# Optimization experiments

Measured on AMD Instinct MI355X. Metric: run time of the kernel, lower is better.

The kernel has to match this reference:

```python
import jax, jax.numpy as jnp
import numpy as np

CH_IN, CH_OUT, CH, NLAYERS = 40, 9, 64, 10
CH_CLOSE = 2 * CH
KSZ = 9  # stencil hard-coded to 9 in init_weights
H = 0.1


def conv1(X, Ker):
    # F.conv1d(X, Ker, padding=(k-1)//2); Ker: (Cout, Cin, k)
    pad = (Ker.shape[-1] - 1) // 2
    return jax.lax.conv_general_dilated(X, Ker, (1,), [(pad, pad)],
                                        dimension_numbers=('NCH', 'OIH', 'NCH'))


def conv1T(X, Ker):
    # F.conv_transpose1d(X, Ker, padding=(k-1)//2) with stride 1 ==
    # conv1d with swapped in/out channels and flipped taps, padding k-1-(k-1)//2
    k = Ker.shape[-1]
    pad = k - 1 - (k - 1) // 2
    Kt = jnp.flip(jnp.swapaxes(Ker, 0, 1), -1)
    return jax.lax.conv_general_dilated(X, Kt, (1,), [(pad, pad)],
                                        dimension_numbers=('NCH', 'OIH', 'NCH'))


def mean_masked(X, mask, axis, keepdims=False):
    return jnp.sum(X * mask, axis=axis, keepdims=keepdims) / jnp.sum(mask, axis=axis, keepdims=keepdims)


def tr2dist(Y):
    # pairwise distances of columns of Y (B,C,N) -> (B,N,N), per Pfold tr2DistSmall
    k = Y.shape[1]
    Z = Y - jnp.mean(Y, axis=2, keepdims=True)
    n2 = jnp.sum(Z * Z, axis=1)  # (B,N)
    D = n2[:, :, None] + n2[:, None, :] - 2.0 * jnp.einsum('bcn,bcm->bnm', Z, Z)
    D = 3.0 * D / k
    Dr = jnp.maximum(D, 0.0)
    safe = jnp.where(Dr > 0, Dr, 1.0)  # grad-safe sqrt
    return jnp.where(Dr > 0, jnp.sqrt(safe), 0.0)


def get_graph_lap(X, mask, sigma):
    # X: (B,C,N), mask: (B,1,N)
    mm = jnp.einsum('bci,bcj->bij', mask, mask)  # (B,N,N) pair mask
    msum = jnp.sum(mask, axis=2, keepdims=True)
    Xc = X - (jnp.sum(X * mask, axis=2, keepdims=True) / msum) * mask
    Xc = Xc / jnp.sqrt(jnp.sum(Xc * Xc, axis=2, keepdims=True) / msum + 1e-4)
    N = X.shape[2]
    pos = 0.5 * jnp.linspace(0.0, 1.0, N)[None, None, :] * mask  # (B,1,N)
    Xa = jnp.concatenate([Xc, pos], axis=1)
    W = tr2dist(Xa) * mm
    W = jnp.exp(-W / sigma * 10.0) * mm
    Wsum = jnp.sum(W, axis=1)  # (B,N)
    D = Wsum[:, :, None] * jnp.eye(N, dtype=W.dtype)  # diag(Wsum)
    L = D - W
    return 0.5 * (L + jnp.swapaxes(L, 1, 2)), W


def double_sym(Z, Wi, Bi, L, mask):
    A0 = conv1(Z + Bi[0], Wi[0]) * mask
    A0 = (A0 - mean_masked(A0, mask, 2, True)) * mask
    A0 = A0 / jnp.sqrt(jnp.sum(A0 * A0, axis=1, keepdims=True) + 1e-3)
    A1 = (conv1(Z + Bi[1], Wi[1]) @ L) * mask
    A1 = (A1 - mean_masked(A1, mask, 2, True)) * mask
    A1 = A1 / jnp.sqrt(jnp.sum(A1 * A1, axis=1, keepdims=True) + 1e-3)
    A0 = jax.nn.relu(A0)
    A1 = jax.nn.relu(A1)
    A0 = conv1T(A0, Wi[0]) * mask
    A1 = (conv1T(A1, Wi[1]) @ L) * mask
    return A0 + A1


def hypernet_forward(Z, mask, Kopen, Kclose, W, Bias):
    mask = mask[:, None, :]  # (B,1,N)
    Z = jnp.einsum('ci,bin->bcn', Kopen, Z) * mask
    L, _ = get_graph_lap(Z, mask, 10.0)
    for i in range(W.shape[0]):
        if i % 10 == 0:
            L, _ = get_graph_lap(Z, mask, 10.0)
        Z = Z - H * double_sym(Z, W[i], Bias[i], L, mask)
    Z = jnp.einsum('oc,bcn->bon', Kclose, Z) * mask
    dists = jnp.stack([tr2dist(Z[:, 3 * i:3 * i + 3, :]) for i in range(Z.shape[1] // 3)], axis=1)
    return dists, Z  # dists: (B, chan_out//3, N, N)


def setup_inputs() -> dict:
    key = jax.random.key(0)
    ks = jax.random.split(key, 5)
    B, N = 8, 1024
    Z = jax.random.normal(ks[0], (B, CH_IN, N), dtype=jnp.float32)
    mask = jnp.ones((B, N), dtype=jnp.float32)
    so = float(CH) / CH_IN
    Kopen = jax.random.uniform(ks[1], (CH, CH_IN), minval=-so, maxval=so, dtype=jnp.float32)
    sc = float(CH_OUT) / CH
    Kclose = jax.random.uniform(ks[2], (CH_OUT, CH), minval=-sc, maxval=sc, dtype=jnp.float32)
    W = jax.random.uniform(ks[3], (NLAYERS, 2, CH_CLOSE, CH, KSZ), minval=-0.1, maxval=0.1, dtype=jnp.float32)
    Bias = jax.random.uniform(ks[4], (NLAYERS, 2, CH, 1), dtype=jnp.float32) * 0.001
    return {"Z": Z, "mask": mask, "Kopen": Kopen, "Kclose": Kclose, "W": W, "Bias": Bias}


def reference(Z, mask, Kopen, Kclose, W, Bias):
    return hypernet_forward(Z, mask, Kopen, Kclose, W, Bias)
```

## Files before the change

### kernel.cpp

```cpp
#include <hip/hip_runtime.h>
#include <cstddef>

#define BB 8
#define NN 1024
#define CIN 40
#define CH 64
#define CC 128
#define COUT 9
#define KS 9
#define NL 10
#define HSTEP 0.1f
#define SKC 2
#define SKH 4

typedef __attribute__((ext_vector_type(8))) short bf16x8;
typedef __attribute__((ext_vector_type(4))) float f32x4;

__device__ __forceinline__ unsigned short f2bf(float f) {
    union { float f; unsigned u; } v;
    v.f = f;
    unsigned u = v.u;
    u += 0x7FFFu + ((u >> 16) & 1u);
    return (unsigned short)(u >> 16);
}
__device__ __forceinline__ float bf2f(unsigned short h) {
    union { unsigned u; float f; } v;
    v.u = ((unsigned)h) << 16;
    return v.f;
}

__device__ __forceinline__ size_t pk_addr(int lb, int row, int col, int R, int KDv) {
    int chunk = ((lb * (R / 32) + (row >> 5)) * (KDv / 32) + (col >> 5)) * 2 + ((row >> 4) & 1);
    int lane = ((col >> 3) & 3) * 16 + (row & 15);
    return ((size_t)chunk * 64 + lane) * 8 + (col & 7);
}

__device__ __forceinline__ float blockSum(float v, float* red) {
    int tid = threadIdx.x;
    red[tid] = v;
    __syncthreads();
    for (int s = 128; s > 0; s >>= 1) {
        if (tid < s) red[tid] += red[tid + s];
        __syncthreads();
    }
    float r = red[0];
    __syncthreads();
    return r;
}

__global__ __launch_bounds__(256) void k_prep_wbf(const float* __restrict__ Win,
                                                  unsigned short* __restrict__ PKc_h,
                                                  unsigned short* __restrict__ PKc_l,
                                                  unsigned short* __restrict__ PKt_h,
                                                  unsigned short* __restrict__ PKt_l) {
    int idx = blockIdx.x * 256 + threadIdx.x;
    const int total = NL * 2 * CC * CH * KS;
    if (idx >= total) return;
    int k = idx % KS;
    int t = idx / KS;
    int i = t % CH;  t /= CH;
    int o = t % CC;  t /= CC;
    int lb = t;
    float v = Win[idx];
    unsigned short h = f2bf(v);
    unsigned short l = f2bf(v - bf2f(h));
    size_t ac = pk_addr(lb, o, k * 64 + i, CC, 576);
    size_t at = pk_addr(lb, i, (8 - k) * 128 + o, CH, 1152);
    PKc_h[ac] = h;
    PKc_l[ac] = l;
    PKt_h[at] = h;
    PKt_l[at] = l;
}

__global__ __launch_bounds__(256) void k_wpack2(const float* __restrict__ Wg,
                                                unsigned short* __restrict__ dst) {
    int idx = blockIdx.x * 256 + threadIdx.x;
    int lane = idx & 63;
    int t = idx >> 6;
    int fn = t & 1; t >>= 1;
    int ms = t & 31; t >>= 5;
    int nt = t & 31;
    int b = t >> 5;
    int r = lane & 15, g = lane >> 4;
    const float* sp = &Wg[((size_t)b * NN + nt * 32 + fn * 16 + r) * NN + ms * 32 + g * 8];
    float v[8];
    *reinterpret_cast<float4*>(&v[0]) = *reinterpret_cast<const float4*>(sp);
    *reinterpret_cast<float4*>(&v[4]) = *reinterpret_cast<const float4*>(sp + 4);
    unsigned short* dp = dst + (size_t)idx * 8;
#pragma unroll
    for (int j = 0; j < 8; ++j) dp[j] = f2bf(v[j]);
}

__global__ __launch_bounds__(256) void k_prep_bks(const float* __restrict__ Win,
                                                  const float* __restrict__ Bias,
                                                  float* __restrict__ bks) {
    int idx = blockIdx.x * 256 + threadIdx.x;
    const int total = NL * 2 * CC * KS;
    if (idx >= total) return;
    int k = idx % KS;
    int t = idx / KS;
    int o = t % CC;
    int lb = t / CC;
    float s = 0.f;
    for (int i = 0; i < CH; ++i)
        s += Win[(((size_t)lb * CC + o) * CH + i) * KS + k] * Bias[lb * CH + i];
    bks[idx] = s;
}

__global__ __launch_bounds__(256) void k_open(const float* __restrict__ Zin,
                                              const float* __restrict__ mask,
                                              const float* __restrict__ Kop,
                                              float* __restrict__ Zcur) {
    int n = blockIdx.x * 256 + threadIdx.x;
    int c = blockIdx.y, b = blockIdx.z;
    float acc = 0.f;
    for (int i = 0; i < CIN; ++i)
        acc += Kop[c * CIN + i] * Zin[((size_t)b * CIN + i) * NN + n];
    Zcur[((size_t)b * CH + c) * NN + n] = acc * mask[b * NN + n];
}

__global__ __launch_bounds__(256) void k_za(const float* __restrict__ Zcur,
                                            const float* __restrict__ mask,
                                            float* __restrict__ Za) {
    __shared__ float red[256];
    int c = blockIdx.x;
    int b = blockIdx.y;
    int tid = threadIdx.x;
    const float* m = mask + b * NN;
    float x[4], mv[4];
    if (c < CH) {
        const float* src = Zcur + ((size_t)b * CH + c) * NN;
#pragma unroll
        for (int j = 0; j < 4; ++j) { int n = tid * 4 + j; x[j] = src[n]; mv[j] = m[n]; }
    } else {
#pragma unroll
        for (int j = 0; j < 4; ++j) { int n = tid * 4 + j; mv[j] = m[n]; x[j] = 0.5f * ((float)n / 1023.f) * mv[j]; }
    }
    float sm = 0.f, sxm = 0.f;
#pragma unroll
    for (int j = 0; j < 4; ++j) { sm += mv[j]; sxm += x[j] * mv[j]; }
    float msum = blockSum(sm, red);
    float xm = blockSum(sxm, red);
    if (c < CH) {
        float mean = xm / msum;
        float ss = 0.f;
#pragma unroll
        for (int j = 0; j < 4; ++j) { x[j] -= mean * mv[j]; ss += x[j] * x[j]; }
        ss = blockSum(ss, red);
        float sc = rsqrtf(ss / msum + 1e-4f);
#pragma unroll
        for (int j = 0; j < 4; ++j) x[j] *= sc;
    }
    float ps = 0.f;
#pragma unroll
    for (int j = 0; j < 4; ++j) ps += x[j];
    float pm = blockSum(ps, red) / (float)NN;
    float* dst = Za + ((size_t)b * 65 + c) * NN;
#pragma unroll
    for (int j = 0; j < 4; ++j) dst[tid * 4 + j] = x[j] - pm;
}

__global__ __launch_bounds__(256) void k_n2g(const float* __restrict__ Za, float* __restrict__ n2g) {
    int n = blockIdx.x * 256 + threadIdx.x;
    int b = blockIdx.y;
    float s = 0.f;
    for (int c = 0; c < 65; ++c) { float v = Za[((size_t)b * 65 + c) * NN + n]; s += v * v; }
    n2g[b * NN + n] = s;
}

__global__ __launch_bounds__(256) void k_gramW(const float* __restrict__ Za,
                                               const float* __restrict__ n2g,
                                               const float* __restrict__ mask,
                                               float* __restrict__ Wg) {
    __shared__ float As[65][64];
    __shared__ float Bs2[65][64];
    int i0 = blockIdx.x * 64, j0 = blockIdx.y * 64, b = blockIdx.z;
    int tid = threadIdx.x;
    for (int e = tid; e < 65 * 64; e += 256) {
        int c = e >> 6, t = e & 63;
        const float* src = Za + ((size_t)b * 65 + c) * NN;
        As[c][t] = src[i0 + t];
        Bs2[c][t] = src[j0 + t];
    }
    __syncthreads();
    int tx = tid & 15, ty = tid >> 4;
    float acc[4][4] = {};
    for (int c = 0; c < 65; ++c) {
        float a[4];
#pragma unroll
        for (int q = 0; q < 4; ++q) a[q] = As[c][ty * 4 + q];
        float bv[4];
        *reinterpret_cast<float4*>(bv) = *reinterpret_cast<const float4*>(&Bs2[c][tx * 4]);
#pragma unroll
        for (int q = 0; q < 4; ++q)
#pragma unroll
            for (int r = 0; r < 4; ++r) acc[q][r] += a[q] * bv[r];
    }
    const float* m = mask + b * NN;
    for (int q = 0; q < 4; ++q) {
        int i = i0 + ty * 4 + q;
        float n2i = n2g[b * NN + i], mi = m[i];
        float res[4];
#pragma unroll
        for (int r = 0; r < 4; ++r) {
            int j = j0 + tx * 4 + r;
            float D = n2i + n2g[b * NN + j] - 2.f * acc[q][r];
            D *= (3.f / 65.f);
            D = fmaxf(D, 0.f);
            float dist = (D > 0.f) ? sqrtf(D) : 0.f;
            float mmv = mi * m[j];
            res[r] = expf(-dist * mmv) * mmv;
        }
        *reinterpret_cast<float4*>(&Wg[((size_t)b * NN + i) * NN + j0 + tx * 4]) =
            *reinterpret_cast<float4*>(res);
    }
}

__global__ __launch_bounds__(256) void k_wsum_part(const float* __restrict__ Wg,
                                                   float* __restrict__ Wsp) {
    int j = blockIdx.x * 256 + threadIdx.x;
    int ch = blockIdx.y;
    int b = blockIdx.z;
    float s = 0.f;
    int i0 = ch * 64;
#pragma unroll 8
    for (int i = 0; i < 64; ++i) s += Wg[((size_t)b * NN + i0 + i) * NN + j];
    Wsp[((size_t)b * 16 + ch) * NN + j] = s;
}
__global__ __launch_bounds__(256) void k_wsum_fin(const float* __restrict__ Wsp,
                                                  float* __restrict__ Wsum) {
    int j = blockIdx.x * 256 + threadIdx.x;
    int b = blockIdx.y;
    float s = 0.f;
#pragma unroll
    for (int ch = 0; ch < 16; ++ch) s += Wsp[((size_t)b * 16 + ch) * NN + j];
    Wsum[b * NN + j] = s;
}

__global__ __launch_bounds__(256) void k_conv1_mfma(const float* __restrict__ Zcur,
                                                    const unsigned short* __restrict__ Wh,
                                                    const unsigned short* __restrict__ Wl,
                                                    const float* __restrict__ bksl,
                                                    const float* __restrict__ mask,
                                                    float* __restrict__ C0,
                                                    float* __restrict__ C1) {
    __shared__ __align__(16) unsigned short xh[80][64];
    __shared__ __align__(16) unsigned short xl[80][64];
    int n0 = blockIdx.x * 64;
    int y = blockIdx.y;
    int b = blockIdx.z;
    int br = y >> 1, half = y & 1;
    int tid = threadIdx.x;
    const float* Xb = Zcur + (size_t)b * CH * NN;

    for (int e = tid; e < 64 * 20; e += 256) {
        int i = e / 20, t = e - i * 20;
        int gn = n0 + t * 4 - 4;
        float4 v = make_float4(0.f, 0.f, 0.f, 0.f);
        if (gn >= 0 && gn + 3 < NN) v = *reinterpret_cast<const float4*>(&Xb[(size_t)i * NN + gn]);
        float vv[4] = {v.x, v.y, v.z, v.w};
#pragma unroll
        for (int j = 0; j < 4; ++j) {
            int row = t * 4 + j;
            int col = i ^ ((row & 7) << 3);
            unsigned short h = f2bf(vv[j]);
            xh[row][col] = h;
            xl[row][col] = f2bf(vv[j] - bf2f(h));
        }
    }
    __syncthreads();

    int wid = tid >> 6, lane = tid & 63;
    int wo = (wid >> 1) * 32, wn = (wid & 1) * 32;
    int r = lane & 15, g = lane >> 4;
    int r32 = half * 2 + (wid >> 1);
    size_t brOff = (size_t)br * (CC / 32) * (576 / 32) * 1024;

    f32x4 acc[2][2] = {};
#pragma unroll 3
    for (int q = 0; q < 18; ++q) {
        int k = q >> 1, s = q & 1;
        size_t widx = brOff + ((size_t)(r32 * 18 + q)) * 1024 + lane * 8;
        bf16x8 ah[2], al[2];
        ah[0] = *reinterpret_cast<const bf16x8*>(&Wh[widx]);
        ah[1] = *reinterpret_cast<const bf16x8*>(&Wh[widx + 512]);
        al[0] = *reinterpret_cast<const bf16x8*>(&Wl[widx]);
        al[1] = *reinterpret_cast<const bf16x8*>(&Wl[widx + 512]);
        bf16x8 bh[2], bl[2];
#pragma unroll
        for (int fn = 0; fn < 2; ++fn) {
            int row = wn + fn * 16 + r + k;
            int chs = (s * 32 + g * 8) ^ ((row & 7) << 3);
            bh[fn] = *reinterpret_cast<const bf16x8*>(&xh[row][chs]);
            bl[fn] = *reinterpret_cast<const bf16x8*>(&xl[row][chs]);
        }
#pragma unroll
        for (int fc = 0; fc < 2; ++fc)
#pragma unroll
            for (int fn = 0; fn < 2; ++fn) {
                acc[fc][fn] = __builtin_amdgcn_mfma_f32_16x16x32_bf16(ah[fc], bh[fn], acc[fc][fn], 0, 0, 0);
                acc[fc][fn] = __builtin_amdgcn_mfma_f32_16x16x32_bf16(al[fc], bh[fn], acc[fc][fn], 0, 0, 0);
                acc[fc][fn] = __builtin_amdgcn_mfma_f32_16x16x32_bf16(ah[fc], bl[fn], acc[fc][fn], 0, 0, 0);
            }
    }

    const float* mkB = mask + b * NN;
    float* Outp = (br ? C1 : C0) + ((size_t)b * CC + half * 64) * NN;
    const float* bo_base = bksl + (br * CC + half * 64) * KS;
#pragma unroll
    for (int fc = 0; fc < 2; ++fc) {
#pragma unroll
        for (int fn = 0; fn < 2; ++fn) {
            int n = n0 + wn + fn * 16 + r;
#pragma unroll
            for (int rr = 0; rr < 4; ++rr) {
                int oo = wo + fc * 16 + 4 * g + rr;
                float v = acc[fc][fn][rr];
                const float* bo = bo_base + oo * KS;
                float bias = 0.f;
#pragma unroll
                for (int k = 0; k < KS; ++k) {
                    int nn2 = n + k - 4;
                    if (nn2 >= 0 && nn2 < NN) bias += bo[k];
                }
                v += bias;
                if (br == 0) v *= mkB[n];
                Outp[(size_t)oo * NN + n] = v;
            }
        }
    }
}

__global__ __launch_bounds__(256) void k_convT_mfma(const float* __restrict__ C0,
                                                    const float* __restrict__ A1,
                                                    const unsigned short* __restrict__ Wh,
                                                    const unsigned short* __restrict__ Wl,
                                                    const float* __restrict__ mask,
                                                    const float* __restrict__ meanA,
                                                    const float* __restrict__ invA,
                                                    float* __restrict__ T0,
                                                    float* __restrict__ T1p) {
    __shared__ __align__(16) unsigned short xh[48][128];
    __shared__ __align__(16) unsigned short xl[48][128];
    __shared__ float red2[2][32][33];
    int n0 = blockIdx.x * 32;
    int br = blockIdx.y;
    int b = blockIdx.z;
    int tid = threadIdx.x;
    const float* Xb = (br ? A1 : C0) + (size_t)b * CC * NN;
    const float* meB = meanA + ((size_t)br * BB + b) * CC;
    const float* ivB = invA + ((size_t)br * BB + b) * NN;
    const float* mkB = mask + b * NN;

    for (int e = tid; e < 128 * 12; e += 256) {
        int i = e / 12, t = e - i * 12;
        int gn = n0 + t * 4 - 4;
        float4 v = make_float4(0.f, 0.f, 0.f, 0.f);
        if (gn >= 0 && gn + 3 < NN) {
            v = *reinterpret_cast<const float4*>(&Xb[(size_t)i * NN + gn]);
            float me = meB[i];
            float4 iv = *reinterpret_cast<const float4*>(&ivB[gn]);
            float4 mk = *reinterpret_cast<const float4*>(&mkB[gn]);
            v.x = fmaxf((v.x - me) * mk.x * iv.x, 0.f);
            v.y = fmaxf((v.y - me) * mk.y * iv.y, 0.f);
            v.z = fmaxf((v.z - me) * mk.z * iv.z, 0.f);
            v.w = fmaxf((v.w - me) * mk.w * iv.w, 0.f);
        }
        float vv[4] = {v.x, v.y, v.z, v.w};
#pragma unroll
        for (int j = 0; j < 4; ++j) {
            int row = t * 4 + j;
            int col = i ^ ((row & 7) << 3);
            unsigned short h = f2bf(vv[j]);
            xh[row][col] = h;
            xl[row][col] = f2bf(vv[j] - bf2f(h));
        }
    }
    __syncthreads();

    int wid = tid >> 6, lane = tid & 63;
    int i32 = wid & 1, kh = wid >> 1;
    int r = lane & 15, g = lane >> 4;
    size_t brW = (size_t)br * (CH / 32) * (1152 / 32) * 1024;

    f32x4 acc[2][2] = {};
#pragma unroll 3
    for (int t = 0; t < 18; ++t) {
        int k = t >> 1, s = kh * 2 + (t & 1);
        int q32 = k * 4 + s;
        size_t widx = brW + ((size_t)(i32 * 36 + q32)) * 1024 + lane * 8;
        bf16x8 ah[2], al[2];
        ah[0] = *reinterpret_cast<const bf16x8*>(&Wh[widx]);
        ah[1] = *reinterpret_cast<const bf16x8*>(&Wh[widx + 512]);
        al[0] = *reinterpret_cast<const bf16x8*>(&Wl[widx]);
        al[1] = *reinterpret_cast<const bf16x8*>(&Wl[widx + 512]);
        bf16x8 bh[2], bl[2];
#pragma unroll
        for (int fn = 0; fn < 2; ++fn) {
            int row = fn * 16 + r + k;
            int chs = (s * 32 + g * 8) ^ ((row & 7) << 3);
            bh[fn] = *reinterpret_cast<const bf16x8*>(&xh[row][chs]);
            bl[fn] = *reinterpret_cast<const bf16x8*>(&xl[row][chs]);
        }
#pragma unroll
        for (int fc = 0; fc < 2; ++fc)
#pragma unroll
            for (int fn = 0; fn < 2; ++fn) {
                acc[fc][fn] = __builtin_amdgcn_mfma_f32_16x16x32_bf16(ah[fc], bh[fn], acc[fc][fn], 0, 0, 0);
                acc[fc][fn] = __builtin_amdgcn_mfma_f32_16x16x32_bf16(al[fc], bh[fn], acc[fc][fn], 0, 0, 0);
                acc[fc][fn] = __builtin_amdgcn_mfma_f32_16x16x32_bf16(ah[fc], bl[fn], acc[fc][fn], 0, 0, 0);
            }
    }

    if (kh == 1) {
#pragma unroll
        for (int fc = 0; fc < 2; ++fc)
#pragma unroll
            for (int fn = 0; fn < 2; ++fn)
#pragma unroll
                for (int rr = 0; rr < 4; ++rr)
                    red2[i32][fc * 16 + 4 * g + rr][fn * 16 + r] = acc[fc][fn][rr];
    }
    __syncthreads();
    if (kh == 0) {
        float* Outp = (br ? T1p : T0) + (size_t)b * CH * NN;
#pragma unroll
        for (int fc = 0; fc < 2; ++fc)
#pragma unroll
            for (int fn = 0; fn < 2; ++fn) {
                int n = n0 + fn * 16 + r;
#pragma unroll
                for (int rr = 0; rr < 4; ++rr) {
                    int irow = fc * 16 + 4 * g + rr;
                    float v = acc[fc][fn][rr] + red2[i32][irow][fn * 16 + r];
                    Outp[(size_t)(i32 * 32 + irow) * NN + n] = v;
                }
            }
    }
}

template <int SKN>
__global__ __launch_bounds__(256) void k_matL_mfma(const float* __restrict__ X,
                                                   const unsigned short* __restrict__ Wpk,
                                                   float* __restrict__ Part, int rows) {
    __shared__ __align__(16) unsigned short Xs[64][36];
    int cb = rows >> 6;
    int n0 = blockIdx.x * 64;
    int sk = blockIdx.y;
    int b = blockIdx.z / cb;
    int c0 = (blockIdx.z % cb) * 64;
    int tid = threadIdx.x;
    int wid = tid >> 6, lane = tid & 63;
    int wc = (wid >> 1) * 32;
    int r = lane & 15, g = lane >> 4;
    const float* Xb = X + (size_t)b * rows * NN;
    int nt32 = blockIdx.x * 2 + (wid & 1);
    const unsigned short* Wb = Wpk + ((size_t)b * 32 + nt32) * 32 * 1024;

    int srow = tid >> 2, scol = (tid & 3) * 8;
    f32x4 acc[2][2] = {};
    int m_beg = sk * (NN / SKN);
    for (int m0 = m_beg; m0 < m_beg + NN / SKN; m0 += 32) {
        {
            const float* sp = &Xb[(size_t)(c0 + srow) * NN + m0 + scol];
            float v[8];
            *reinterpret_cast<float4*>(&v[0]) = *reinterpret_cast<const float4*>(sp);
            *reinterpret_cast<float4*>(&v[4]) = *reinterpret_cast<const float4*>(sp + 4);
            unsigned short h[8];
#pragma unroll
            for (int j = 0; j < 8; ++j) h[j] = f2bf(v[j]);
            *reinterpret_cast<ushort4*>(&Xs[srow][scol]) = *reinterpret_cast<ushort4*>(&h[0]);
            *reinterpret_cast<ushort4*>(&Xs[srow][scol + 4]) = *reinterpret_cast<ushort4*>(&h[4]);
        }
        __syncthreads();
        bf16x8 afr[2];
#pragma unroll
        for (int fc = 0; fc < 2; ++fc) {
            const uint2* p = reinterpret_cast<const uint2*>(&Xs[wc + fc * 16 + r][8 * g]);
            uint2 q0 = p[0], q1 = p[1];
            union { unsigned int u[4]; bf16x8 v; } ua;
            ua.u[0] = q0.x; ua.u[1] = q0.y; ua.u[2] = q1.x; ua.u[3] = q1.y;
            afr[fc] = ua.v;
        }
        size_t wb = (size_t)(m0 >> 5) * 1024 + lane * 8;
        bf16x8 bfr[2];
        bfr[0] = *reinterpret_cast<const bf16x8*>(&Wb[wb]);
        bfr[1] = *reinterpret_cast<const bf16x8*>(&Wb[wb + 512]);
#pragma unroll
        for (int fc = 0; fc < 2; ++fc)
#pragma unroll
            for (int fn = 0; fn < 2; ++fn)
                acc[fc][fn] = __builtin_amdgcn_mfma_f32_16x16x32_bf16(afr[fc], bfr[fn], acc[fc][fn], 0, 0, 0);
        __syncthreads();
    }
    int wn = (wid & 1) * 32;
#pragma unroll
    for (int fc = 0; fc < 2; ++fc)
#pragma unroll
        for (int fn = 0; fn < 2; ++fn) {
            int ncol = n0 + wn + fn * 16 + r;
#pragma unroll
            for (int rr = 0; rr < 4; ++rr) {
                int crow = c0 + wc + fc * 16 + 4 * g + rr;
                Part[(((size_t)b * SKN + sk) * rows + crow) * NN + ncol] = acc[fc][fn][rr];
            }
        }
}

template <int SKN, int MODE>
__global__ __launch_bounds__(256) void k_matL_fin(const float* __restrict__ X,
                                                  const float* __restrict__ Part,
                                                  const float* __restrict__ Wsum,
                                                  const float* __restrict__ mask,
                                                  const float* __restrict__ T0,
                                                  float* __restrict__ Out,
                                                  float* __restrict__ meanA, int rows) {
    __shared__ float red[256];
    int c = blockIdx.x, b = blockIdx.y;
    int n = threadIdx.x * 4;
    float4 s = make_float4(0.f, 0.f, 0.f, 0.f);
#pragma unroll
    for (int sk = 0; sk < SKN; ++sk) {
        float4 p = *reinterpret_cast<const float4*>(
            &Part[(((size_t)b * SKN + sk) * rows + c) * NN + n]);
        s.x += p.x; s.y += p.y; s.z += p.z; s.w += p.w;
    }
    float4 xv = *reinterpret_cast<const float4*>(&X[((size_t)b * rows + c) * NN + n]);
    float4 wv = *reinterpret_cast<const float4*>(&Wsum[b * NN + n]);
    float4 mv = *reinterpret_cast<const float4*>(&mask[b * NN + n]);
    float y0 = xv.x * wv.x - s.x, y1 = xv.y * wv.y - s.y;
    float y2 = xv.z * wv.z - s.z, y3 = xv.w * wv.w - s.w;
    if (MODE == 0) {
        float4 res = make_float4(y0 * mv.x, y1 * mv.y, y2 * mv.z, y3 * mv.w);
        *reinterpret_cast<float4*>(&Out[((size_t)b * rows + c) * NN + n]) = res;
        float rs = res.x * mv.x + res.y * mv.y + res.z * mv.z + res.w * mv.w;
        float ms = mv.x + mv.y + mv.z + mv.w;
        rs = blockSum(rs, red);
        ms = blockSum(ms, red);
        if (threadIdx.x == 0) meanA[((size_t)BB + b) * CC + c] = rs / ms;
    } else {
        float4 t0 = *reinterpret_cast<const float4*>(&T0[((size_t)b * rows + c) * NN + n]);
        float4 o = *reinterpret_cast<const float4*>(&Out[((size_t)b * rows + c) * NN + n]);
        float4 res = make_float4(o.x - HSTEP * mv.x * (t0.x + y0),
                                 o.y - HSTEP * mv.y * (t0.y + y1),
                                 o.z - HSTEP * mv.z * (t0.z + y2),
                                 o.w - HSTEP * mv.w * (t0.w + y3));
        *reinterpret_cast<float4*>(&Out[((size_t)b * rows + c) * NN + n]) = res;
    }
}

__global__ __launch_bounds__(256) void k_rowmean(const float* __restrict__ X0,
                                                 const float* __restrict__ mask,
                                                 float* __restrict__ meanA) {
    __shared__ float red[256];
    int c = blockIdx.x, b = blockIdx.y, tid = threadIdx.x;
    const float* src = X0 + ((size_t)b * CC + c) * NN;
    const float* m = mask + b * NN;
    float s = 0.f, sm = 0.f;
    for (int n = tid; n < NN; n += 256) { float mv = m[n]; s += src[n] * mv; sm += mv; }
    float ts = blockSum(s, red);
    float tm = blockSum(sm, red);
    if (tid == 0) meanA[(size_t)b * CC + c] = ts / tm;
}

__global__ __launch_bounds__(256) void k_colnorm_inv(const float* __restrict__ X0,
                                                     const float* __restrict__ X1,
                                                     const float* __restrict__ mask,
                                                     const float* __restrict__ meanA,
                                                     float* __restrict__ invA) {
    __shared__ float red[8][32];
    int tid = threadIdx.x;
    int nl = tid & 31, cg = tid >> 5;
    int n = blockIdx.x * 32 + nl;
    int b = blockIdx.y, z = blockIdx.z;
    const float* X = (z ? X1 : X0) + (size_t)b * CC * NN;
    const float* me = meanA + ((size_t)z * BB + b) * CC;
    float mv = mask[b * NN + n];
    float ss = 0.f;
#pragma unroll
    for (int cc = 0; cc < 16; ++cc) {
        int c = cg * 16 + cc;
        float v = (X[(size_t)c * NN + n] - me[c]) * mv;
        ss += v * v;
    }
    red[cg][nl] = ss;
    __syncthreads();
    if (cg < 4) red[cg][nl] += red[cg + 4][nl];
    __syncthreads();
    if (cg < 2) red[cg][nl] += red[cg + 2][nl];
    __syncthreads();
    if (cg < 1) red[0][nl] += red[1][nl];
    __syncthreads();
    if (cg == 0) invA[((size_t)z * BB + b) * NN + n] = rsqrtf(red[0][nl] + 0.001f);
}

__global__ __launch_bounds__(256) void k_close(const float* __restrict__ Zcur,
                                               const float* __restrict__ Kcl,
                                               const float* __restrict__ mask,
                                               float* __restrict__ Zout) {
    __shared__ float red[4][64][COUT];
    int tid = threadIdx.x;
    int nl = tid & 63, cg = tid >> 6;
    int n = blockIdx.x * 64 + nl;
    int b = blockIdx.y;
    float acc[COUT] = {};
#pragma unroll
    for (int cc = 0; cc < 16; ++cc) {
        int c = cg * 16 + cc;
        float zv = Zcur[((size_t)b * CH + c) * NN + n];
#pragma unroll
        for (int o = 0; o < COUT; ++o) acc[o] += Kcl[o * CH + c] * zv;
    }
#pragma unroll
    for (int o = 0; o < COUT; ++o) red[cg][nl][o] = acc[o];
    __syncthreads();
    if (cg == 0) {
        float mv = mask[b * NN + n];
#pragma unroll
        for (int o = 0; o < COUT; ++o) {
            float s = red[0][nl][o] + red[1][nl][o] + red[2][nl][o] + red[3][nl][o];
            Zout[((size_t)b * COUT + o) * NN + n] = s * mv;
        }
    }
}

__global__ __launch_bounds__(256) void k_center3(const float* __restrict__ Zout, float* __restrict__ Zc3) {
    __shared__ float red[256];
    int c = blockIdx.x, b = blockIdx.y, tid = threadIdx.x;
    const float* src = Zout + ((size_t)b * COUT + c) * NN;
    float s = 0.f;
    for (int n = tid; n < NN; n += 256) s += src[n];
    float mean = blockSum(s, red) / (float)NN;
    float* dst = Zc3 + ((size_t)b * COUT + c) * NN;
    for (int n = tid; n < NN; n += 256) dst[n] = src[n] - mean;
}

__global__ __launch_bounds__(256) void k_n23(const float* __restrict__ Zc3, float* __restrict__ n23) {
    int n = blockIdx.x * 256 + threadIdx.x;
    int g = blockIdx.y, b = blockIdx.z;
    float s = 0.f;
#pragma unroll
    for (int c = 0; c < 3; ++c) { float v = Zc3[((size_t)b * COUT + g * 3 + c) * NN + n]; s += v * v; }
    n23[((size_t)b * 3 + g) * NN + n] = s;
}

__global__ __launch_bounds__(256) void k_dist(const float* __restrict__ Zc3,
                                              const float* __restrict__ n23,
                                              float* __restrict__ dout) {
    __shared__ float Ai[3][64], Aj[3][64], ni[64], nj[64];
    int bg = blockIdx.z;
    int b = bg / 3, g = bg - 3 * b;
    int i0 = blockIdx.x * 64, j0 = blockIdx.y * 64;
    int tid = threadIdx.x;
    if (tid < 64) ni[tid] = n23[((size_t)b * 3 + g) * NN + i0 + tid];
    else if (tid < 128) { int t = tid - 64; nj[t] = n23[((size_t)b * 3 + g) * NN + j0 + t]; }
    for (int e = tid; e < 192; e += 256) {
        int c = e / 64, t = e - c * 64;
        Ai[c][t] = Zc3[((size_t)b * COUT + g * 3 + c) * NN + i0 + t];
    }
    for (int e = tid; e < 192; e += 256) {
        int c = e / 64, t = e - c * 64;
        Aj[c][t] = Zc3[((size_t)b * COUT + g * 3 + c) * NN + j0 + t];
    }
    __syncthreads();
    int tx = tid & 15, ty = tid >> 4;
    for (int q = 0; q < 4; ++q) {
        int i = ty * 4 + q;
        float a0 = Ai[0][i], a1 = Ai[1][i], a2 = Ai[2][i], n2i = ni[i];
        float res[4];
#pragma unroll
        for (int r = 0; r < 4; ++r) {
            int j = tx * 4 + r;
            float D = n2i + nj[j] - 2.f * (a0 * Aj[0][j] + a1 * Aj[1][j] + a2 * Aj[2][j]);
            D = fmaxf(D, 0.f);
            res[r] = (D > 0.f) ? sqrtf(D) : 0.f;
        }
        *reinterpret_cast<float4*>(&dout[(((size_t)b * 3 + g) * NN + i0 + i) * NN + j0 + tx * 4]) =
            *reinterpret_cast<float4*>(res);
    }
}

extern "C" void kernel_launch(void* const* d_in, const int* in_sizes, int n_in,
                              void* d_out, int out_size, void* d_ws, size_t ws_size,
                              hipStream_t stream) {
    (void)in_sizes; (void)n_in; (void)out_size; (void)ws_size;
    const float* Zin  = (const float*)d_in[0];
    const float* mask = (const float*)d_in[1];
    const float* Kop  = (const float*)d_in[2];
    const float* Kcl  = (const float*)d_in[3];
    const float* Win  = (const float*)d_in[4];
    const float* Bias = (const float*)d_in[5];
    float* out = (float*)d_out;
    float* ws = (float*)d_ws;

    size_t off = 0;
    float* Zcur = ws + off;  off += (size_t)BB * CH * NN;
    float* C0   = ws + off;  off += (size_t)BB * CC * NN;
    float* C1   = ws + off;  off += (size_t)BB * CC * NN;
    float* A1   = ws + off;  off += (size_t)BB * CC * NN;
    float* T0   = ws + off;  off += (size_t)BB * CH * NN;
    float* T1p  = ws + off;  off += (size_t)BB * CH * NN;
    float* Za   = ws + off;  off += (size_t)BB * 65 * NN;
    float* n2g  = ws + off;  off += (size_t)BB * NN;
    float* Wg   = ws + off;  off += (size_t)BB * NN * NN;
    float* Wsum = ws + off;  off += (size_t)BB * NN;
    float* meanA= ws + off;  off += (size_t)2 * BB * CC;
    float* bks  = ws + off;  off += (size_t)NL * 2 * CC * KS;
    float* Zc3  = ws + off;  off += (size_t)BB * COUT * NN;
    float* n23  = ws + off;  off += (size_t)BB * 3 * NN;
    float* Wsp  = ws + off;  off += (size_t)BB * 16 * NN;
    float* invA = ws + off;  off += (size_t)2 * BB * NN;

    float* Part = out;
    unsigned short* Wpk2  = (unsigned short*)(out + (size_t)4194304);
    unsigned short* PKc_h = (unsigned short*)(out + (size_t)14680064);
    unsigned short* PKc_l = (unsigned short*)(out + (size_t)15417344);
    unsigned short* PKt_h = (unsigned short*)(out + (size_t)16154624);
    unsigned short* PKt_l = (unsigned short*)(out + (size_t)16891904);

    const int wtot = NL * 2 * CC * CH * KS;
    k_prep_wbf<<<dim3((wtot + 255) / 256), 256, 0, stream>>>(Win, PKc_h, PKc_l, PKt_h, PKt_l);
    k_prep_bks<<<dim3((NL * 2 * CC * KS + 255) / 256), 256, 0, stream>>>(Win, Bias, bks);
    k_open<<<dim3(NN / 256, CH, BB), 256, 0, stream>>>(Zin, mask, Kop, Zcur);
    k_za<<<dim3(65, BB), 256, 0, stream>>>(Zcur, mask, Za);
    k_n2g<<<dim3(NN / 256, BB), 256, 0, stream>>>(Za, n2g);
    k_gramW<<<dim3(16, 16, BB), 256, 0, stream>>>(Za, n2g, mask, Wg);
    k_wsum_part<<<dim3(NN / 256, 16, BB), 256, 0, stream>>>(Wg, Wsp);
    k_wsum_fin<<<dim3(NN / 256, BB), 256, 0, stream>>>(Wsp, Wsum);
    k_wpack2<<<dim3((int)((size_t)BB * NN * NN / 8 / 256)), 256, 0, stream>>>(Wg, Wpk2);

    for (int l = 0; l < NL; ++l) {
        const unsigned short* PKc_h_l = PKc_h + (size_t)l * 2 * CC * 576;
        const unsigned short* PKc_l_l = PKc_l + (size_t)l * 2 * CC * 576;
        const unsigned short* PKt_h_l = PKt_h + (size_t)l * 2 * CH * 1152;
        const unsigned short* PKt_l_l = PKt_l + (size_t)l * 2 * CH * 1152;
        const float* bksl = bks + (size_t)l * 2 * CC * KS;

        k_conv1_mfma<<<dim3(NN / 64, 4, BB), 256, 0, stream>>>(
            Zcur, PKc_h_l, PKc_l_l, bksl, mask, C0, C1);
        k_matL_mfma<SKC><<<dim3(NN / 64, SKC, BB * (CC / 64)), 256, 0, stream>>>(C1, Wpk2, Part, CC);
        k_matL_fin<SKC, 0><<<dim3(CC, BB), 256, 0, stream>>>(
            C1, Part, Wsum, mask, nullptr, A1, meanA, CC);
        k_rowmean<<<dim3(CC, BB), 256, 0, stream>>>(C0, mask, meanA);
        k_colnorm_inv<<<dim3(NN / 32, BB, 2), 256, 0, stream>>>(C0, A1, mask, meanA, invA);
        k_convT_mfma<<<dim3(NN / 32, 2, BB), 256, 0, stream>>>(
            C0, A1, PKt_h_l, PKt_l_l, mask, meanA, invA, T0, T1p);
        k_matL_mfma<SKH><<<dim3(NN / 64, SKH, BB * (CH / 64)), 256, 0, stream>>>(T1p, Wpk2, Part, CH);
        k_matL_fin<SKH, 1><<<dim3(CH, BB), 256, 0, stream>>>(
            T1p, Part, Wsum, mask, T0, Zcur, nullptr, CH);
    }

    float* Zout = out + (size_t)BB * 3 * NN * NN;
    k_close<<<dim3(NN / 64, BB), 256, 0, stream>>>(Zcur, Kcl, mask, Zout);
    k_center3<<<dim3(COUT, BB), 256, 0, stream>>>(Zout, Zc3);
    k_n23<<<dim3(NN / 256, 3, BB), 256, 0, stream>>>(Zc3, n23);
    k_dist<<<dim3(16, 16, 3 * BB), 256, 0, stream>>>(Zc3, n23, out);
}
```

Before: 952.2 us.

## Fuse graph weight packing and column sums into gram kernel; prepack matL operands

The gram kernel now writes the bf16 MFMA-packed W matrix and accumulates column sums with atomics, instead of storing a full fp32 W and running separate wsum and pack kernels. The conv1 and convT kernels also emit bf16 fragment-packed copies of C1 and T1p, so matL loads its A-operand directly from global memory without LDS staging or syncs. This removes a 32MB fp32 write and read plus several launches, and makes the inner matL loop pure loads and MFMAs. In exchange there are extra scattered 2-byte stores in the conv epilogues, and atomic adds make the column-sum order nondeterministic.

```diff
diff --git a/kernel.cpp b/kernel.cpp
--- a/kernel.cpp
+++ b/kernel.cpp
@@ -46,6 +46,11 @@
     float r = red[0];
     __syncthreads();
     return r;
+}
+
+__global__ __launch_bounds__(256) void k_zero(float* __restrict__ p, int n) {
+    int i = blockIdx.x * 256 + threadIdx.x;
+    if (i < n) p[i] = 0.f;
 }
 
 __global__ __launch_bounds__(256) void k_prep_wbf(const float* __restrict__ Win,
@@ -72,25 +77,6 @@
     PKt_l[at] = l;
 }
 
-__global__ __launch_bounds__(256) void k_wpack2(const float* __restrict__ Wg,
-                                                unsigned short* __restrict__ dst) {
-    int idx = blockIdx.x * 256 + threadIdx.x;
-    int lane = idx & 63;
-    int t = idx >> 6;
-    int fn = t & 1; t >>= 1;
-    int ms = t & 31; t >>= 5;
-    int nt = t & 31;
-    int b = t >> 5;
-    int r = lane & 15, g = lane >> 4;
-    const float* sp = &Wg[((size_t)b * NN + nt * 32 + fn * 16 + r) * NN + ms * 32 + g * 8];
-    float v[8];
-    *reinterpret_cast<float4*>(&v[0]) = *reinterpret_cast<const float4*>(sp);
-    *reinterpret_cast<float4*>(&v[4]) = *reinterpret_cast<const float4*>(sp + 4);
-    unsigned short* dp = dst + (size_t)idx * 8;
-#pragma unroll
-    for (int j = 0; j < 8; ++j) dp[j] = f2bf(v[j]);
-}
-
 __global__ __launch_bounds__(256) void k_prep_bks(const float* __restrict__ Win,
                                                   const float* __restrict__ Bias,
                                                   float* __restrict__ bks) {
@@ -171,9 +157,12 @@
 __global__ __launch_bounds__(256) void k_gramW(const float* __restrict__ Za,
                                                const float* __restrict__ n2g,
                                                const float* __restrict__ mask,
-                                               float* __restrict__ Wg) {
+                                               unsigned short* __restrict__ Wpk,
+                                               float* __restrict__ Wsum) {
     __shared__ float As[65][64];
     __shared__ float Bs2[65][64];
+    __shared__ unsigned short wt[64][72];
+    __shared__ float csred[16][64];
     int i0 = blockIdx.x * 64, j0 = blockIdx.y * 64, b = blockIdx.z;
     int tid = threadIdx.x;
     for (int e = tid; e < 65 * 64; e += 256) {
@@ -197,10 +186,10 @@
             for (int r = 0; r < 4; ++r) acc[q][r] += a[q] * bv[r];
     }
     const float* m = mask + b * NN;
+    float csacc[4] = {0.f, 0.f, 0.f, 0.f};
     for (int q = 0; q < 4; ++q) {
         int i = i0 + ty * 4 + q;
         float n2i = n2g[b * NN + i], mi = m[i];
-        float res[4];
 #pragma unroll
         for (int r = 0; r < 4; ++r) {
             int j = j0 + tx * 4 + r;
@@ -209,32 +198,35 @@
             D = fmaxf(D, 0.f);
             float dist = (D > 0.f) ? sqrtf(D) : 0.f;
             float mmv = mi * m[j];
-            res[r] = expf(-dist * mmv) * mmv;
-        }
-        *reinterpret_cast<float4*>(&Wg[((size_t)b * NN + i) * NN + j0 + tx * 4]) =
-            *reinterpret_cast<float4*>(res);
-    }
-}
-
-__global__ __launch_bounds__(256) void k_wsum_part(const float* __restrict__ Wg,
-                                                   float* __restrict__ Wsp) {
-    int j = blockIdx.x * 256 + threadIdx.x;
-    int ch = blockIdx.y;
-    int b = blockIdx.z;
-    float s = 0.f;
-    int i0 = ch * 64;
-#pragma unroll 8
-    for (int i = 0; i < 64; ++i) s += Wg[((size_t)b * NN + i0 + i) * NN + j];
-    Wsp[((size_t)b * 16 + ch) * NN + j] = s;
-}
-__global__ __launch_bounds__(256) void k_wsum_fin(const float* __restrict__ Wsp,
-                                                  float* __restrict__ Wsum) {
-    int j = blockIdx.x * 256 + threadIdx.x;
-    int b = blockIdx.y;
-    float s = 0.f;
-#pragma unroll
-    for (int ch = 0; ch < 16; ++ch) s += Wsp[((size_t)b * 16 + ch) * NN + j];
-    Wsum[b * NN + j] = s;
+            float res = expf(-dist * mmv) * mmv;
+            wt[ty * 4 + q][tx * 4 + r] = f2bf(res);
+            csacc[r] += res;
+        }
+    }
+#pragma unroll
+    for (int r = 0; r < 4; ++r) csred[ty][tx * 4 + r] = csacc[r];
+    __syncthreads();
+    for (int s = 8; s > 0; s >>= 1) {
+        if (ty < s) {
+#pragma unroll
+            for (int r = 0; r < 4; ++r) csred[ty][tx * 4 + r] += csred[ty + s][tx * 4 + r];
+        }
+        __syncthreads();
+    }
+    if (ty == 0) {
+#pragma unroll
+        for (int r = 0; r < 4; ++r)
+            atomicAdd(&Wsum[b * NN + j0 + tx * 4 + r], csred[0][tx * 4 + r]);
+    }
+    for (int e = tid; e < 512; e += 256) {
+        int li = e >> 3, ljb = (e & 7) * 8;
+        int row = i0 + li, col = j0 + ljb;
+        int chunk = ((b * 32 + (row >> 5)) * 32 + (col >> 5)) * 2 + ((row >> 4) & 1);
+        int lane2 = ((col >> 3) & 3) * 16 + (row & 15);
+        unsigned short* dp = Wpk + ((size_t)chunk * 64 + lane2) * 8;
+        *reinterpret_cast<ushort4*>(dp) = *reinterpret_cast<ushort4*>(&wt[li][ljb]);
+        *reinterpret_cast<ushort4*>(dp + 4) = *reinterpret_cast<ushort4*>(&wt[li][ljb + 4]);
+    }
 }
 
 __global__ __launch_bounds__(256) void k_conv1_mfma(const float* __restrict__ Zcur,
@@ -243,7 +235,8 @@
                                                     const float* __restrict__ bksl,
                                                     const float* __restrict__ mask,
                                                     float* __restrict__ C0,
-                                                    float* __restrict__ C1) {
+                                                    float* __restrict__ C1,
+                                                    unsigned short* __restrict__ C1pk) {
     __shared__ __align__(16) unsigned short xh[80][64];
     __shared__ __align__(16) unsigned short xl[80][64];
     int n0 = blockIdx.x * 64;
@@ -326,6 +319,12 @@
                 v += bias;
                 if (br == 0) v *= mkB[n];
                 Outp[(size_t)oo * NN + n] = v;
+                if (br == 1) {
+                    int cg = half * 64 + oo;
+                    int chunk = ((b * 4 + (cg >> 5)) * 32 + (n >> 5)) * 2 + ((cg >> 4) & 1);
+                    int lane2 = ((n >> 3) & 3) * 16 + (cg & 15);
+                    C1pk[((size_t)chunk * 64 + lane2) * 8 + (n & 7)] = f2bf(v);
+                }
             }
         }
     }
@@ -339,7 +338,8 @@
                                                     const float* __restrict__ meanA,
                                                     const float* __restrict__ invA,
                                                     float* __restrict__ T0,
-                                                    float* __restrict__ T1p) {
+                                                    float* __restrict__ T1p,
+                                                    unsigned short* __restrict__ T1pk) {
     __shared__ __align__(16) unsigned short xh[48][128];
     __shared__ __align__(16) unsigned short xl[48][128];
     __shared__ float red2[2][32][33];
@@ -434,18 +434,22 @@
                     int irow = fc * 16 + 4 * g + rr;
                     float v = acc[fc][fn][rr] + red2[i32][irow][fn * 16 + r];
                     Outp[(size_t)(i32 * 32 + irow) * NN + n] = v;
+                    if (br == 1) {
+                        int cg = i32 * 32 + irow;
+                        int chunk = ((b * 2 + (cg >> 5)) * 32 + (n >> 5)) * 2 + ((cg >> 4) & 1);
+                        int lane2 = ((n >> 3) & 3) * 16 + (cg & 15);
+                        T1pk[((size_t)chunk * 64 + lane2) * 8 + (n & 7)] = f2bf(v);
+                    }
                 }
             }
     }
 }
 
 template <int SKN>
-__global__ __launch_bounds__(256) void k_matL_mfma(const float* __restrict__ X,
+__global__ __launch_bounds__(256) void k_matL_mfma(const unsigned short* __restrict__ Xpk,
                                                    const unsigned short* __restrict__ Wpk,
                                                    float* __restrict__ Part, int rows) {
-    __shared__ __align__(16) unsigned short Xs[64][36];
     int cb = rows >> 6;
-    int n0 = blockIdx.x * 64;
     int sk = blockIdx.y;
     int b = blockIdx.z / cb;
     int c0 = (blockIdx.z % cb) * 64;
@@ -453,46 +457,26 @@
     int wid = tid >> 6, lane = tid & 63;
     int wc = (wid >> 1) * 32;
     int r = lane & 15, g = lane >> 4;
-    const float* Xb = X + (size_t)b * rows * NN;
+    int rowsT = rows >> 5;
+    int ct = (c0 >> 5) + (wid >> 1);
     int nt32 = blockIdx.x * 2 + (wid & 1);
-    const unsigned short* Wb = Wpk + ((size_t)b * 32 + nt32) * 32 * 1024;
-
-    int srow = tid >> 2, scol = (tid & 3) * 8;
+    const unsigned short* Xb = Xpk + ((size_t)(b * rowsT + ct)) * 32768 + (size_t)lane * 8;
+    const unsigned short* Wb = Wpk + ((size_t)(b * 32 + nt32)) * 32768 + (size_t)lane * 8;
+
     f32x4 acc[2][2] = {};
-    int m_beg = sk * (NN / SKN);
-    for (int m0 = m_beg; m0 < m_beg + NN / SKN; m0 += 32) {
-        {
-            const float* sp = &Xb[(size_t)(c0 + srow) * NN + m0 + scol];
-            float v[8];
-            *reinterpret_cast<float4*>(&v[0]) = *reinterpret_cast<const float4*>(sp);
-            *reinterpret_cast<float4*>(&v[4]) = *reinterpret_cast<const float4*>(sp + 4);
-            unsigned short h[8];
-#pragma unroll
-            for (int j = 0; j < 8; ++j) h[j] = f2bf(v[j]);
-            *reinterpret_cast<ushort4*>(&Xs[srow][scol]) = *reinterpret_cast<ushort4*>(&h[0]);
-            *reinterpret_cast<ushort4*>(&Xs[srow][scol + 4]) = *reinterpret_cast<ushort4*>(&h[4]);
-        }
-        __syncthreads();
-        bf16x8 afr[2];
-#pragma unroll
-        for (int fc = 0; fc < 2; ++fc) {
-            const uint2* p = reinterpret_cast<const uint2*>(&Xs[wc + fc * 16 + r][8 * g]);
-            uint2 q0 = p[0], q1 = p[1];
-            union { unsigned int u[4]; bf16x8 v; } ua;
-            ua.u[0] = q0.x; ua.u[1] = q0.y; ua.u[2] = q1.x; ua.u[3] = q1.y;
-            afr[fc] = ua.v;
-        }
-        size_t wb = (size_t)(m0 >> 5) * 1024 + lane * 8;
-        bf16x8 bfr[2];
-        bfr[0] = *reinterpret_cast<const bf16x8*>(&Wb[wb]);
-        bfr[1] = *reinterpret_cast<const bf16x8*>(&Wb[wb + 512]);
-#pragma unroll
-        for (int fc = 0; fc < 2; ++fc)
-#pragma unroll
-            for (int fn = 0; fn < 2; ++fn)
-                acc[fc][fn] = __builtin_amdgcn_mfma_f32_16x16x32_bf16(afr[fc], bfr[fn], acc[fc][fn], 0, 0, 0);
-        __syncthreads();
-    }
+    int ms_beg = sk * (32 / SKN);
+#pragma unroll 4
+    for (int ms = ms_beg; ms < ms_beg + 32 / SKN; ++ms) {
+        bf16x8 a0 = *reinterpret_cast<const bf16x8*>(&Xb[(size_t)ms * 1024]);
+        bf16x8 a1 = *reinterpret_cast<const bf16x8*>(&Xb[(size_t)ms * 1024 + 512]);
+        bf16x8 w0 = *reinterpret_cast<const bf16x8*>(&Wb[(size_t)ms * 1024]);
+        bf16x8 w1 = *reinterpret_cast<const bf16x8*>(&Wb[(size_t)ms * 1024 + 512]);
+        acc[0][0] = __builtin_amdgcn_mfma_f32_16x16x32_bf16(a0, w0, acc[0][0], 0, 0, 0);
+        acc[0][1] = __builtin_amdgcn_mfma_f32_16x16x32_bf16(a0, w1, acc[0][1], 0, 0, 0);
+        acc[1][0] = __builtin_amdgcn_mfma_f32_16x16x32_bf16(a1, w0, acc[1][0], 0, 0, 0);
+        acc[1][1] = __builtin_amdgcn_mfma_f32_16x16x32_bf16(a1, w1, acc[1][1], 0, 0, 0);
+    }
+    int n0 = blockIdx.x * 64;
     int wn = (wid & 1) * 32;
 #pragma unroll
     for (int fc = 0; fc < 2; ++fc)
@@ -702,17 +686,17 @@
     float* T1p  = ws + off;  off += (size_t)BB * CH * NN;
     float* Za   = ws + off;  off += (size_t)BB * 65 * NN;
     float* n2g  = ws + off;  off += (size_t)BB * NN;
-    float* Wg   = ws + off;  off += (size_t)BB * NN * NN;
     float* Wsum = ws + off;  off += (size_t)BB * NN;
     float* meanA= ws + off;  off += (size_t)2 * BB * CC;
     float* bks  = ws + off;  off += (size_t)NL * 2 * CC * KS;
     float* Zc3  = ws + off;  off += (size_t)BB * COUT * NN;
     float* n23  = ws + off;  off += (size_t)BB * 3 * NN;
-    float* Wsp  = ws + off;  off += (size_t)BB * 16 * NN;
     float* invA = ws + off;  off += (size_t)2 * BB * NN;
 
     float* Part = out;
     unsigned short* Wpk2  = (unsigned short*)(out + (size_t)4194304);
+    unsigned short* C1pk  = (unsigned short*)(out + (size_t)8388608);
+    unsigned short* T1pk  = (unsigned short*)(out + (size_t)8912896);
     unsigned short* PKc_h = (unsigned short*)(out + (size_t)14680064);
     unsigned short* PKc_l = (unsigned short*)(out + (size_t)15417344);
     unsigned short* PKt_h = (unsigned short*)(out + (size_t)16154624);
@@ -721,13 +705,11 @@
     const int wtot = NL * 2 * CC * CH * KS;
     k_prep_wbf<<<dim3((wtot + 255) / 256), 256, 0, stream>>>(Win, PKc_h, PKc_l, PKt_h, PKt_l);
     k_prep_bks<<<dim3((NL * 2 * CC * KS + 255) / 256), 256, 0, stream>>>(Win, Bias, bks);
+    k_zero<<<dim3(BB * NN / 256), 256, 0, stream>>>(Wsum, BB * NN);
     k_open<<<dim3(NN / 256, CH, BB), 256, 0, stream>>>(Zin, mask, Kop, Zcur);
     k_za<<<dim3(65, BB), 256, 0, stream>>>(Zcur, mask, Za);
     k_n2g<<<dim3(NN / 256, BB), 256, 0, stream>>>(Za, n2g);
-    k_gramW<<<dim3(16, 16, BB), 256, 0, stream>>>(Za, n2g, mask, Wg);
-    k_wsum_part<<<dim3(NN / 256, 16, BB), 256, 0, stream>>>(Wg, Wsp);
-    k_wsum_fin<<<dim3(NN / 256, BB), 256, 0, stream>>>(Wsp, Wsum);
-    k_wpack2<<<dim3((int)((size_t)BB * NN * NN / 8 / 256)), 256, 0, stream>>>(Wg, Wpk2);
+    k_gramW<<<dim3(16, 16, BB), 256, 0, stream>>>(Za, n2g, mask, Wpk2, Wsum);
 
     for (int l = 0; l < NL; ++l) {
         const unsigned short* PKc_h_l = PKc_h + (size_t)l * 2 * CC * 576;
@@ -737,15 +719,15 @@
         const float* bksl = bks + (size_t)l * 2 * CC * KS;
 
         k_conv1_mfma<<<dim3(NN / 64, 4, BB), 256, 0, stream>>>(
-            Zcur, PKc_h_l, PKc_l_l, bksl, mask, C0, C1);
-        k_matL_mfma<SKC><<<dim3(NN / 64, SKC, BB * (CC / 64)), 256, 0, stream>>>(C1, Wpk2, Part, CC);
+            Zcur, PKc_h_l, PKc_l_l, bksl, mask, C0, C1, C1pk);
+        k_matL_mfma<SKC><<<dim3(NN / 64, SKC, BB * (CC / 64)), 256, 0, stream>>>(C1pk, Wpk2, Part, CC);
         k_matL_fin<SKC, 0><<<dim3(CC, BB), 256, 0, stream>>>(
             C1, Part, Wsum, mask, nullptr, A1, meanA, CC);
         k_rowmean<<<dim3(CC, BB), 256, 0, stream>>>(C0, mask, meanA);
         k_colnorm_inv<<<dim3(NN / 32, BB, 2), 256, 0, stream>>>(C0, A1, mask, meanA, invA);
         k_convT_mfma<<<dim3(NN / 32, 2, BB), 256, 0, stream>>>(
-            C0, A1, PKt_h_l, PKt_l_l, mask, meanA, invA, T0, T1p);
-        k_matL_mfma<SKH><<<dim3(NN / 64, SKH, BB * (CH / 64)), 256, 0, stream>>>(T1p, Wpk2, Part, CH);
+            C0, A1, PKt_h_l, PKt_l_l, mask, meanA, invA, T0, T1p, T1pk);
+        k_matL_mfma<SKH><<<dim3(NN / 64, SKH, BB * (CH / 64)), 256, 0, stream>>>(T1pk, Wpk2, Part, CH);
         k_matL_fin<SKH, 1><<<dim3(CH, BB), 256, 0, stream>>>(
             T1p, Part, Wsum, mask, T0, Zcur, nullptr, CH);
     }
```

After: 869.1 us. -8.7%, faster.
